# Kernel optimization log

Hardware: AMD Instinct MI355X
Metric: run time of the kernel (lower is better)

## Reference

```python
import jax, jax.numpy as jnp
import numpy as np
import math

N_HEAD = 4
NORM_GROUPS = 32
EPS = 1e-5


def setup_inputs() -> dict:
    key = jax.random.key(0)
    ks = jax.random.split(key, 6)
    C = 256
    x = jax.random.normal(ks[0], (2, C, 64, 64), dtype=jnp.float32)
    gn_w = jnp.ones((C,), dtype=jnp.float32)
    gn_b = jnp.zeros((C,), dtype=jnp.float32)
    s = 1.0 / math.sqrt(C)
    wq = jax.random.normal(ks[1], (C, C), dtype=jnp.float32) * s
    wk = jax.random.normal(ks[2], (C, C), dtype=jnp.float32) * s
    wv = jax.random.normal(ks[3], (C, C), dtype=jnp.float32) * s
    wo = jax.random.normal(ks[4], (C, C), dtype=jnp.float32) * s
    bo = jnp.zeros((C,), dtype=jnp.float32)
    return {"x": x, "gn_w": gn_w, "gn_b": gn_b, "wq": wq, "wk": wk,
            "wv": wv, "wo": wo, "bo": bo}


def group_norm(x, w, b):
    bsz, c, h, wd = x.shape
    xg = x.reshape(bsz, NORM_GROUPS, c // NORM_GROUPS, h, wd)
    mu = jnp.mean(xg, axis=(2, 3, 4), keepdims=True)
    var = jnp.mean(jnp.square(xg - mu), axis=(2, 3, 4), keepdims=True)
    xn = ((xg - mu) * jax.lax.rsqrt(var + EPS)).reshape(bsz, c, h, wd)
    return xn * w[None, :, None, None] + b[None, :, None, None]


def conv1x1(x, w):
    # w: (out_ch, in_ch) applied pointwise
    return jnp.einsum('bchw,oc->bohw', x, w)


def reference(x, gn_w, gn_b, wq, wk, wv, wo, bo):
    bsz, c, h, w = x.shape
    hd = c // N_HEAD
    norm = group_norm(x, gn_w, gn_b)
    q = conv1x1(norm, wq).reshape(bsz, N_HEAD, hd, h, w)
    k = conv1x1(norm, wk).reshape(bsz, N_HEAD, hd, h, w)
    v = conv1x1(norm, wv).reshape(bsz, N_HEAD, hd, h, w)
    # scores over full spatial positions; NOTE: scaled by sqrt(channel), as in source
    scores = jnp.einsum('bnchw,bncxy->bnhwxy', q, k) / jnp.sqrt(jnp.float32(c))
    probs = jax.nn.softmax(scores.reshape(bsz, N_HEAD, h, w, h * w), axis=-1)
    probs = probs.reshape(bsz, N_HEAD, h, w, h, w)
    out = jnp.einsum('bnhwxy,bncxy->bnchw', probs, v).reshape(bsz, c, h, w)
    out = conv1x1(out, wo) + bo[None, :, None, None]
    return out + x
```

## Files before the change

### kernel.cpp

```cpp
#include <hip/hip_runtime.h>

typedef float f32x4 __attribute__((ext_vector_type(4)));
typedef float f32x16 __attribute__((ext_vector_type(16)));
typedef short bf16x8 __attribute__((ext_vector_type(8)));
typedef unsigned short u16;
typedef unsigned int u32;

#define MFMA(a, b, c) __builtin_amdgcn_mfma_f32_16x16x32_bf16((a), (b), (c), 0, 0, 0)
#define MFMA32(a, b, c) __builtin_amdgcn_mfma_f32_32x32x16_bf16((a), (b), (c), 0, 0, 0)

static __device__ __forceinline__ u16 f2bf(float f) {
    union { float f; u32 u; } v; v.f = f;
    u32 r = v.u + 0x7FFFu + ((v.u >> 16) & 1u);
    return (u16)(r >> 16);
}

static __device__ __forceinline__ u32 pkbf(float a, float b) {
    u32 ua = __float_as_uint(a) + 0x8000u;
    u32 ub = __float_as_uint(b) + 0x8000u;
    return __builtin_amdgcn_perm(ub, ua, 0x07060302);
}

__global__ __launch_bounds__(256) void wcvt_kernel(
    const float* __restrict__ wq, const float* __restrict__ wk,
    const float* __restrict__ wv, const float* __restrict__ wo,
    u16* __restrict__ Wbf) {
    int base = (blockIdx.x * 256 + threadIdx.x) * 4;
    int p = base >> 16;
    int off = base & 65535;
    const float* W = (p == 0) ? wq : ((p == 1) ? wk : ((p == 2) ? wv : wo));
    float sc = (p == 0) ? 0.0625f : 1.0f;
    float4 v = *(const float4*)(W + off);
    uint2 pk;
    pk.x = pkbf(v.x * sc, v.y * sc);
    pk.y = pkbf(v.z * sc, v.w * sc);
    *(uint2*)(Wbf + base) = pk;
}

__global__ __launch_bounds__(256) void gn_stats(
    const float* __restrict__ x, float2* __restrict__ part) {
    int blk = blockIdx.x;
    int bg = blk >> 2, quarter = blk & 3;
    const float* xp = x + (size_t)bg * 32768 + quarter * 8192;
    int t = threadIdx.x;

    float s = 0.f, ss = 0.f;
#pragma unroll
    for (int rep = 0; rep < 8; ++rep) {
        float4 v = *(const float4*)(xp + t * 4 + rep * 1024);
        s += v.x + v.y + v.z + v.w;
        ss += v.x * v.x + v.y * v.y + v.z * v.z + v.w * v.w;
    }
    for (int off = 1; off < 64; off <<= 1) {
        s += __shfl_xor(s, off);
        ss += __shfl_xor(ss, off);
    }
    __shared__ float red[8];
    int lane = t & 63, w = t >> 6;
    if (lane == 0) { red[w] = s; red[4 + w] = ss; }
    __syncthreads();
    if (t == 0) {
        part[blk] = make_float2(red[0] + red[1] + red[2] + red[3],
                                red[4] + red[5] + red[6] + red[7]);
    }
}

__global__ __launch_bounds__(256) void gn_apply(
    const float* __restrict__ x, const float* __restrict__ gw,
    const float* __restrict__ gb, const float2* __restrict__ part,
    u16* __restrict__ normT) {
    int s0 = blockIdx.x * 32;
    int b = blockIdx.y;
    int t = threadIdx.x;
    __shared__ u16 tile[32 * 264];
    __shared__ float2 gstat[32];

    if (t < 32) {
        float s = 0.f, ss = 0.f;
#pragma unroll
        for (int q = 0; q < 4; ++q) {
            float2 p = part[(b * 32 + t) * 4 + q];
            s += p.x; ss += p.y;
        }
        float mu = s * (1.f / 32768.f);
        float var = ss * (1.f / 32768.f) - mu * mu;
        gstat[t] = make_float2(mu, rsqrtf(var + 1e-5f));
    }
    __syncthreads();

    int sj = (t & 7) * 4;
#pragma unroll
    for (int i = 0; i < 8; ++i) {
        int c = (t >> 3) + 32 * i;
        float2 st = gstat[c >> 3];
        float wgt = gw[c] * st.y;
        float bia = gb[c] - st.x * wgt;
        float4 v = *(const float4*)(x + (size_t)(b * 256 + c) * 4096 + s0 + sj);
        tile[(sj + 0) * 264 + c] = f2bf(v.x * wgt + bia);
        tile[(sj + 1) * 264 + c] = f2bf(v.y * wgt + bia);
        tile[(sj + 2) * 264 + c] = f2bf(v.z * wgt + bia);
        tile[(sj + 3) * 264 + c] = f2bf(v.w * wgt + bia);
    }
    __syncthreads();
#pragma unroll
    for (int k = 0; k < 4; ++k) {
        int idx = t + 256 * k;
        int row = idx >> 5, ch = idx & 31;
        *(uint4*)(normT + ((size_t)(b * 4096 + s0 + row)) * 256 + ch * 8) =
            *(const uint4*)(tile + row * 264 + ch * 8);
    }
}

__global__ __launch_bounds__(256) void qkv_gemm(
    const u16* __restrict__ normT, const u16* __restrict__ Wbf,
    u16* __restrict__ Q, u16* __restrict__ K, u16* __restrict__ V) {
    int b = blockIdx.y & 1;
    int p = blockIdx.y >> 1;
    const u16* W = Wbf + p * 65536;
    int m0 = (blockIdx.x & 1) * 128;
    int n0 = (blockIdx.x >> 1) * 64;

    __shared__ u16 a_s[128 * 40];
    __shared__ u16 b_s[64 * 40];

    int t = threadIdx.x;
    int lane = t & 63, wave = t >> 6;
    int wm = wave & 1, wn = wave >> 1;
    int r = lane & 15, qd = lane >> 4;

    const u16* Bsrc = normT + (size_t)b * 4096 * 256;

    f32x4 acc[4][2];
#pragma unroll
    for (int i = 0; i < 4; ++i)
#pragma unroll
        for (int j = 0; j < 2; ++j) acc[i][j] = (f32x4){0.f, 0.f, 0.f, 0.f};

    int srow = t >> 1;
    int scp = (t & 1) * 16;

    for (int kk = 0; kk < 256; kk += 32) {
        __syncthreads();
        {
            const u16* src = W + (m0 + srow) * 256 + kk + scp;
            *(uint4*)(a_s + srow * 40 + scp) = *(const uint4*)(src);
            *(uint4*)(a_s + srow * 40 + scp + 8) = *(const uint4*)(src + 8);
        }
        if (t < 128) {
            const u16* src = Bsrc + (size_t)(n0 + srow) * 256 + kk + scp;
            *(uint4*)(b_s + srow * 40 + scp) = *(const uint4*)(src);
            *(uint4*)(b_s + srow * 40 + scp + 8) = *(const uint4*)(src + 8);
        }
        __syncthreads();

        bf16x8 af[4], bf[2];
#pragma unroll
        for (int mt = 0; mt < 4; ++mt)
            af[mt] = *(const bf16x8*)(a_s + (wm * 64 + mt * 16 + r) * 40 + qd * 8);
#pragma unroll
        for (int nt = 0; nt < 2; ++nt)
            bf[nt] = *(const bf16x8*)(b_s + (wn * 32 + nt * 16 + r) * 40 + qd * 8);
        if (p == 2) {
#pragma unroll
            for (int mt = 0; mt < 4; ++mt)
#pragma unroll
                for (int nt = 0; nt < 2; ++nt)
                    acc[mt][nt] = MFMA(bf[nt], af[mt], acc[mt][nt]);
        } else {
#pragma unroll
            for (int mt = 0; mt < 4; ++mt)
#pragma unroll
                for (int nt = 0; nt < 2; ++nt)
                    acc[mt][nt] = MFMA(af[mt], bf[nt], acc[mt][nt]);
        }
    }

    if (p < 2) {
        u16* dst = (p == 0) ? Q : K;
#pragma unroll
        for (int mt = 0; mt < 4; ++mt) {
#pragma unroll
            for (int nt = 0; nt < 2; ++nt) {
                int o0 = m0 + wm * 64 + mt * 16 + qd * 4;
                int s = n0 + wn * 32 + nt * 16 + r;
                int h = o0 >> 6, d0 = o0 & 63;
                uint2 pk;
                pk.x = pkbf(acc[mt][nt][0], acc[mt][nt][1]);
                pk.y = pkbf(acc[mt][nt][2], acc[mt][nt][3]);
                *(uint2*)(dst + ((size_t)((b * 4 + h) * 4096 + s)) * 64 + d0) = pk;
            }
        }
    } else {
#pragma unroll
        for (int mt = 0; mt < 4; ++mt) {
#pragma unroll
            for (int nt = 0; nt < 2; ++nt) {
                int o = m0 + wm * 64 + mt * 16 + r;
                int h = o >> 6, d = o & 63;
                int sb = n0 + wn * 32 + nt * 16 + qd * 4;
                uint2 pk;
                pk.x = pkbf(acc[mt][nt][0], acc[mt][nt][1]);
                pk.y = pkbf(acc[mt][nt][2], acc[mt][nt][3]);
                *(uint2*)(V + ((size_t)((b * 4 + h) * 64 + d)) * 4096 + sb) = pk;
            }
        }
    }
}

template <int QT>
__global__ __launch_bounds__(256, 2) void attn_kernel(
    const u16* __restrict__ Q, const u16* __restrict__ K,
    const u16* __restrict__ V, u16* __restrict__ Opart,
    float* __restrict__ Lpart, int nk32) {
    int bh = blockIdx.x & 7, sp = blockIdx.x >> 3;
    int qb = blockIdx.y;
    int t = threadIdx.x, lane = t & 63, w = t >> 6;
    int qn = lane & 31, h = lane >> 5;

    const size_t bhoff = (size_t)bh * 4096 * 64;
    int q0 = (qb * 4 + w) * (32 * QT);
    int kbase = sp * nk32 * 32;

    bf16x8 qf[QT][4];
#pragma unroll
    for (int qt = 0; qt < QT; ++qt)
#pragma unroll
        for (int c = 0; c < 4; ++c)
            qf[qt][c] = *(const bf16x8*)(Q + bhoff +
                (size_t)(q0 + qt * 32 + qn) * 64 + c * 16 + h * 8);

    f32x16 oacc[2][QT];
#pragma unroll
    for (int dt = 0; dt < 2; ++dt)
#pragma unroll
        for (int qt = 0; qt < QT; ++qt)
#pragma unroll
            for (int i = 0; i < 16; ++i) oacc[dt][qt][i] = 0.f;
    float lacc[QT];
#pragma unroll
    for (int qt = 0; qt < QT; ++qt) lacc[qt] = 0.f;

    const u16* Kp = K + bhoff;
    const u16* Vp = V + bhoff;

    for (int kt = 0; kt < nk32; ++kt) {
        int k0 = kbase + kt * 32;
        bf16x8 kf[4];
#pragma unroll
        for (int c = 0; c < 4; ++c)
            kf[c] = *(const bf16x8*)(Kp + (size_t)(k0 + qn) * 64 + c * 16 + h * 8);
        bf16x8 vf[2][2];
#pragma unroll
        for (int dt = 0; dt < 2; ++dt)
#pragma unroll
            for (int kc = 0; kc < 2; ++kc)
                vf[dt][kc] = *(const bf16x8*)(Vp +
                    (size_t)(dt * 32 + qn) * 4096 + k0 + kc * 16 + h * 8);

#pragma unroll
        for (int qt = 0; qt < QT; ++qt) {
            f32x16 s;
#pragma unroll
            for (int i = 0; i < 16; ++i) s[i] = 0.f;
#pragma unroll
            for (int c = 0; c < 4; ++c) s = MFMA32(kf[c], qf[qt][c], s);

            float e[16];
            float ls = 0.f;
#pragma unroll
            for (int i = 0; i < 16; ++i) { e[i] = __expf(s[i]); ls += e[i]; }
            lacc[qt] += ls;

            u32 p[8], rm[8];
#pragma unroll
            for (int i = 0; i < 8; ++i) p[i] = pkbf(e[2 * i], e[2 * i + 1]);
#pragma unroll
            for (int i = 0; i < 8; ++i)
                rm[i] = (u32)__shfl_xor((int)p[i], 32);

            u32 a0 = h ? rm[2] : p[0], a1 = h ? rm[3] : p[1];
            u32 a2 = h ? p[2] : rm[0], a3 = h ? p[3] : rm[1];
            u32 b0 = h ? rm[6] : p[4], b1 = h ? rm[7] : p[5];
            u32 b2 = h ? p[6] : rm[4], b3 = h ? p[7] : rm[5];
            uint4 pau = {a0, a1, a2, a3};
            uint4 pbu = {b0, b1, b2, b3};
            bf16x8 pA = *(const bf16x8*)&pau;
            bf16x8 pB = *(const bf16x8*)&pbu;

#pragma unroll
            for (int dt = 0; dt < 2; ++dt) {
                oacc[dt][qt] = MFMA32(vf[dt][0], pA, oacc[dt][qt]);
                oacc[dt][qt] = MFMA32(vf[dt][1], pB, oacc[dt][qt]);
            }
        }
    }

    float lfull[QT];
#pragma unroll
    for (int qt = 0; qt < QT; ++qt)
        lfull[qt] = lacc[qt] + __shfl_xor(lacc[qt], 32);

    __shared__ u16 osw[4][64 * 72];
    u16* my = osw[w];
#pragma unroll
    for (int qt = 0; qt < QT; ++qt) {
        int row = qt * 32 + qn;
#pragma unroll
        for (int dt = 0; dt < 2; ++dt) {
#pragma unroll
            for (int g = 0; g < 4; ++g) {
                int d0 = g * 8 + h * 4 + dt * 32;
                uint2 pk;
                pk.x = pkbf(oacc[dt][qt][4 * g], oacc[dt][qt][4 * g + 1]);
                pk.y = pkbf(oacc[dt][qt][4 * g + 2], oacc[dt][qt][4 * g + 3]);
                *(uint2*)(my + row * 72 + d0) = pk;
            }
        }
    }
    __syncthreads();

    size_t obase = ((size_t)sp * 8 + bh) * 4096 + q0;
#pragma unroll
    for (int rr = 0; rr < 4 * QT; ++rr) {
        int row = rr * 8 + (lane >> 3), ch = lane & 7;
        uint4 v = *(const uint4*)(my + row * 72 + ch * 8);
        *(uint4*)(Opart + (obase + row) * 64 + ch * 8) = v;
    }
    if (h == 0) {
#pragma unroll
        for (int qt = 0; qt < QT; ++qt)
            Lpart[obase + qt * 32 + qn] = lfull[qt];
    }
}

__global__ __launch_bounds__(256) void attn_combine(
    const u16* __restrict__ Opart, const float* __restrict__ Lpart,
    u16* __restrict__ attnT, int nsplit) {
    int t = threadIdx.x;
    int gr = blockIdx.x * 64 + (t >> 2);
    int d0 = (t & 3) * 16;

    float l = 0.f;
    for (int s = 0; s < nsplit; ++s) l += Lpart[(size_t)s * 32768 + gr];
    float inv = 1.f / l;

    float acc[16];
#pragma unroll
    for (int i = 0; i < 16; ++i) acc[i] = 0.f;
    for (int s = 0; s < nsplit; ++s) {
        const u16* p = Opart + ((size_t)s * 32768 + gr) * 64 + d0;
        uint4 a = *(const uint4*)(p);
        uint4 bq = *(const uint4*)(p + 8);
        const u32* ap = (const u32*)&a;
        const u32* bp = (const u32*)&bq;
#pragma unroll
        for (int j = 0; j < 4; ++j) {
            acc[2 * j]     += __uint_as_float(ap[j] << 16);
            acc[2 * j + 1] += __uint_as_float(ap[j] & 0xFFFF0000u);
            acc[8 + 2 * j]     += __uint_as_float(bp[j] << 16);
            acc[8 + 2 * j + 1] += __uint_as_float(bp[j] & 0xFFFF0000u);
        }
    }
    u32 pk[8];
#pragma unroll
    for (int j = 0; j < 8; ++j)
        pk[j] = pkbf(acc[2 * j] * inv, acc[2 * j + 1] * inv);

    int bh = gr >> 12, q = gr & 4095;
    int b = bh >> 2, hh = bh & 3;
    u16* dst = attnT + ((size_t)(b * 4096 + q)) * 256 + hh * 64 + d0;
    *(uint4*)(dst) = make_uint4(pk[0], pk[1], pk[2], pk[3]);
    *(uint4*)(dst + 8) = make_uint4(pk[4], pk[5], pk[6], pk[7]);
}

__global__ __launch_bounds__(256) void out_gemm(
    const u16* __restrict__ attnT, const u16* __restrict__ W3,
    const float* __restrict__ bo, const float* __restrict__ x,
    float* __restrict__ out) {
    int b = blockIdx.y;
    int m0 = (blockIdx.x & 3) * 64;
    int n0 = (blockIdx.x >> 2) * 64;

    __shared__ u16 a_s[64 * 40];
    __shared__ u16 b_s[64 * 40];

    int t = threadIdx.x;
    int lane = t & 63, wave = t >> 6;
    int wm = wave & 1, wn = wave >> 1;
    int r = lane & 15, qd = lane >> 4;

    const u16* Bsrc = attnT + (size_t)b * 4096 * 256;

    f32x4 acc[2][2];
#pragma unroll
    for (int i = 0; i < 2; ++i)
#pragma unroll
        for (int j = 0; j < 2; ++j) acc[i][j] = (f32x4){0.f, 0.f, 0.f, 0.f};

    int u = t & 127;
    int srow = u >> 1;
    int scp = (u & 1) * 16;

    for (int kk = 0; kk < 256; kk += 32) {
        __syncthreads();
        if (t < 128) {
            const u16* src = W3 + (m0 + srow) * 256 + kk + scp;
            *(uint4*)(a_s + srow * 40 + scp) = *(const uint4*)(src);
            *(uint4*)(a_s + srow * 40 + scp + 8) = *(const uint4*)(src + 8);
        } else {
            const u16* src = Bsrc + (size_t)(n0 + srow) * 256 + kk + scp;
            *(uint4*)(b_s + srow * 40 + scp) = *(const uint4*)(src);
            *(uint4*)(b_s + srow * 40 + scp + 8) = *(const uint4*)(src + 8);
        }
        __syncthreads();

        bf16x8 af[2], bf[2];
#pragma unroll
        for (int mt = 0; mt < 2; ++mt)
            af[mt] = *(const bf16x8*)(a_s + (wm * 32 + mt * 16 + r) * 40 + qd * 8);
#pragma unroll
        for (int nt = 0; nt < 2; ++nt)
            bf[nt] = *(const bf16x8*)(b_s + (wn * 32 + nt * 16 + r) * 40 + qd * 8);
#pragma unroll
        for (int mt = 0; mt < 2; ++mt)
#pragma unroll
            for (int nt = 0; nt < 2; ++nt)
                acc[mt][nt] = MFMA(af[mt], bf[nt], acc[mt][nt]);
    }

#pragma unroll
    for (int mt = 0; mt < 2; ++mt) {
#pragma unroll
        for (int nt = 0; nt < 2; ++nt) {
#pragma unroll
            for (int j = 0; j < 4; ++j) {
                int o = m0 + wm * 32 + mt * 16 + qd * 4 + j;
                int s = n0 + wn * 32 + nt * 16 + r;
                size_t idx = (size_t)(b * 256 + o) * 4096 + s;
                out[idx] = acc[mt][nt][j] + bo[o] + x[idx];
            }
        }
    }
}

extern "C" void kernel_launch(void* const* d_in, const int* in_sizes, int n_in,
                              void* d_out, int out_size, void* d_ws, size_t ws_size,
                              hipStream_t stream) {
    const float* x = (const float*)d_in[0];
    const float* gn_w = (const float*)d_in[1];
    const float* gn_b = (const float*)d_in[2];
    const float* wq = (const float*)d_in[3];
    const float* wk = (const float*)d_in[4];
    const float* wv = (const float*)d_in[5];
    const float* wo = (const float*)d_in[6];
    const float* bo = (const float*)d_in[7];
    float* out = (float*)d_out;

    char* ws = (char*)d_ws;
    u16* normT = (u16*)(ws);
    u16* attnT = (u16*)(ws);
    u16* Q     = (u16*)(ws + (4u << 20));
    u16* Kp    = (u16*)(ws + (8u << 20));
    u16* Vp    = (u16*)(ws + (12u << 20));
    u16* Wbf   = (u16*)(ws + (16u << 20));
    float2* part = (float2*)(ws + (16u << 20) + 524288);

    size_t opart_off = (size_t)17 << 20;
    size_t opart_bytes4 = 4ull * 8 * 4096 * 64 * 2;
    int nsplit = (ws_size >= opart_off + opart_bytes4 + 4ull * 32768 * 4 + 4096)
                     ? 4 : 2;
    u16* Opart = (u16*)(ws + opart_off);
    float* Lpart = (float*)(ws + opart_off + (size_t)nsplit * 8 * 4096 * 64 * 2);

    wcvt_kernel<<<256, 256, 0, stream>>>(wq, wk, wv, wo, Wbf);
    gn_stats<<<256, 256, 0, stream>>>(x, part);
    gn_apply<<<dim3(128, 2), 256, 0, stream>>>(x, gn_w, gn_b, part, normT);
    qkv_gemm<<<dim3(128, 6), 256, 0, stream>>>(normT, Wbf, Q, Kp, Vp);
    if (nsplit == 4) {
        attn_kernel<2><<<dim3(32, 16), 256, 0, stream>>>(Q, Kp, Vp, Opart, Lpart, 32);
    } else {
        attn_kernel<1><<<dim3(16, 32), 256, 0, stream>>>(Q, Kp, Vp, Opart, Lpart, 64);
    }
    attn_combine<<<512, 256, 0, stream>>>(Opart, Lpart, attnT, nsplit);
    out_gemm<<<dim3(256, 2), 256, 0, stream>>>(attnT, Wbf + 3 * 65536, bo, x, out);
}
```

Measured before the change: 172.7 us.

## Fuse weight conversion and split-combine into GEMMs, double-buffer KV loads in attention

Removes the separate weight-conversion kernel by converting fp32 weights to bf16 inside the QKV and output GEMM tile loads. Removes the attn_combine kernel by summing split partial outputs and normalizing inside the output GEMM's B-tile load. In attention, K/V fragments are loaded one step ahead into ping-pong register buffers, and the V load is changed to strided uint2 loads, which removes the cross-lane shuffle that rearranged P. Fewer launches and intermediate buffers are traded for redundant weight conversion per block and extra register pressure.

```diff
diff --git a/kernel.cpp b/kernel.cpp
--- a/kernel.cpp
+++ b/kernel.cpp
@@ -21,20 +21,9 @@
     return __builtin_amdgcn_perm(ub, ua, 0x07060302);
 }
 
-__global__ __launch_bounds__(256) void wcvt_kernel(
-    const float* __restrict__ wq, const float* __restrict__ wk,
-    const float* __restrict__ wv, const float* __restrict__ wo,
-    u16* __restrict__ Wbf) {
-    int base = (blockIdx.x * 256 + threadIdx.x) * 4;
-    int p = base >> 16;
-    int off = base & 65535;
-    const float* W = (p == 0) ? wq : ((p == 1) ? wk : ((p == 2) ? wv : wo));
-    float sc = (p == 0) ? 0.0625f : 1.0f;
-    float4 v = *(const float4*)(W + off);
-    uint2 pk;
-    pk.x = pkbf(v.x * sc, v.y * sc);
-    pk.y = pkbf(v.z * sc, v.w * sc);
-    *(uint2*)(Wbf + base) = pk;
+static __device__ __forceinline__ bf16x8 mk8(uint2 a, uint2 b) {
+    uint4 t = {a.x, a.y, b.x, b.y};
+    return *(const bf16x8*)&t;
 }
 
 __global__ __launch_bounds__(256) void gn_stats(
@@ -112,11 +101,13 @@
 }
 
 __global__ __launch_bounds__(256) void qkv_gemm(
-    const u16* __restrict__ normT, const u16* __restrict__ Wbf,
+    const u16* __restrict__ normT, const float* __restrict__ wq,
+    const float* __restrict__ wk, const float* __restrict__ wv,
     u16* __restrict__ Q, u16* __restrict__ K, u16* __restrict__ V) {
     int b = blockIdx.y & 1;
     int p = blockIdx.y >> 1;
-    const u16* W = Wbf + p * 65536;
+    const float* W = (p == 0) ? wq : ((p == 1) ? wk : wv);
+    float sc = (p == 0) ? 0.0625f : 1.0f;
     int m0 = (blockIdx.x & 1) * 128;
     int n0 = (blockIdx.x >> 1) * 64;
 
@@ -142,9 +133,22 @@
     for (int kk = 0; kk < 256; kk += 32) {
         __syncthreads();
         {
-            const u16* src = W + (m0 + srow) * 256 + kk + scp;
-            *(uint4*)(a_s + srow * 40 + scp) = *(const uint4*)(src);
-            *(uint4*)(a_s + srow * 40 + scp + 8) = *(const uint4*)(src + 8);
+            const float* src = W + (m0 + srow) * 256 + kk + scp;
+            float4 f0 = *(const float4*)(src + 0);
+            float4 f1 = *(const float4*)(src + 4);
+            float4 f2 = *(const float4*)(src + 8);
+            float4 f3 = *(const float4*)(src + 12);
+            uint4 o0, o1;
+            o0.x = pkbf(f0.x * sc, f0.y * sc);
+            o0.y = pkbf(f0.z * sc, f0.w * sc);
+            o0.z = pkbf(f1.x * sc, f1.y * sc);
+            o0.w = pkbf(f1.z * sc, f1.w * sc);
+            o1.x = pkbf(f2.x * sc, f2.y * sc);
+            o1.y = pkbf(f2.z * sc, f2.w * sc);
+            o1.z = pkbf(f3.x * sc, f3.y * sc);
+            o1.w = pkbf(f3.z * sc, f3.w * sc);
+            *(uint4*)(a_s + srow * 40 + scp) = o0;
+            *(uint4*)(a_s + srow * 40 + scp + 8) = o1;
         }
         if (t < 128) {
             const u16* src = Bsrc + (size_t)(n0 + srow) * 256 + kk + scp;
@@ -207,6 +211,25 @@
     }
 }
 
+struct KVfrag {
+    bf16x8 kf[4];
+    bf16x8 vf[2][2];
+};
+
+static __device__ __forceinline__ void load_kv(
+    KVfrag& o, const u16* __restrict__ Kp, const u16* __restrict__ Vp,
+    int k0, int qn, int h) {
+#pragma unroll
+    for (int c = 0; c < 4; ++c)
+        o.kf[c] = *(const bf16x8*)(Kp + (size_t)(k0 + qn) * 64 + c * 16 + h * 8);
+#pragma unroll
+    for (int dt = 0; dt < 2; ++dt) {
+        const u16* vr = Vp + (size_t)(dt * 32 + qn) * 4096 + k0 + 4 * h;
+        o.vf[dt][0] = mk8(*(const uint2*)(vr), *(const uint2*)(vr + 8));
+        o.vf[dt][1] = mk8(*(const uint2*)(vr + 16), *(const uint2*)(vr + 24));
+    }
+}
+
 template <int QT>
 __global__ __launch_bounds__(256, 2) void attn_kernel(
     const u16* __restrict__ Q, const u16* __restrict__ K,
@@ -243,27 +266,17 @@
     const u16* Kp = K + bhoff;
     const u16* Vp = V + bhoff;
 
-    for (int kt = 0; kt < nk32; ++kt) {
-        int k0 = kbase + kt * 32;
-        bf16x8 kf[4];
-#pragma unroll
-        for (int c = 0; c < 4; ++c)
-            kf[c] = *(const bf16x8*)(Kp + (size_t)(k0 + qn) * 64 + c * 16 + h * 8);
-        bf16x8 vf[2][2];
-#pragma unroll
-        for (int dt = 0; dt < 2; ++dt)
-#pragma unroll
-            for (int kc = 0; kc < 2; ++kc)
-                vf[dt][kc] = *(const bf16x8*)(Vp +
-                    (size_t)(dt * 32 + qn) * 4096 + k0 + kc * 16 + h * 8);
-
+    KVfrag buf0, buf1;
+    load_kv(buf0, Kp, Vp, kbase, qn, h);
+
+    auto step = [&](const KVfrag& kv) {
 #pragma unroll
         for (int qt = 0; qt < QT; ++qt) {
             f32x16 s;
 #pragma unroll
             for (int i = 0; i < 16; ++i) s[i] = 0.f;
 #pragma unroll
-            for (int c = 0; c < 4; ++c) s = MFMA32(kf[c], qf[qt][c], s);
+            for (int c = 0; c < 4; ++c) s = MFMA32(kv.kf[c], qf[qt][c], s);
 
             float e[16];
             float ls = 0.f;
@@ -271,28 +284,28 @@
             for (int i = 0; i < 16; ++i) { e[i] = __expf(s[i]); ls += e[i]; }
             lacc[qt] += ls;
 
-            u32 p[8], rm[8];
+            u32 p[8];
 #pragma unroll
             for (int i = 0; i < 8; ++i) p[i] = pkbf(e[2 * i], e[2 * i + 1]);
-#pragma unroll
-            for (int i = 0; i < 8; ++i)
-                rm[i] = (u32)__shfl_xor((int)p[i], 32);
-
-            u32 a0 = h ? rm[2] : p[0], a1 = h ? rm[3] : p[1];
-            u32 a2 = h ? p[2] : rm[0], a3 = h ? p[3] : rm[1];
-            u32 b0 = h ? rm[6] : p[4], b1 = h ? rm[7] : p[5];
-            u32 b2 = h ? p[6] : rm[4], b3 = h ? p[7] : rm[5];
-            uint4 pau = {a0, a1, a2, a3};
-            uint4 pbu = {b0, b1, b2, b3};
-            bf16x8 pA = *(const bf16x8*)&pau;
-            bf16x8 pB = *(const bf16x8*)&pbu;
+            uint4 pa = {p[0], p[1], p[2], p[3]};
+            uint4 pb = {p[4], p[5], p[6], p[7]};
+            bf16x8 pA = *(const bf16x8*)&pa;
+            bf16x8 pB = *(const bf16x8*)&pb;
 
 #pragma unroll
             for (int dt = 0; dt < 2; ++dt) {
-                oacc[dt][qt] = MFMA32(vf[dt][0], pA, oacc[dt][qt]);
-                oacc[dt][qt] = MFMA32(vf[dt][1], pB, oacc[dt][qt]);
+                oacc[dt][qt] = MFMA32(kv.vf[dt][0], pA, oacc[dt][qt]);
+                oacc[dt][qt] = MFMA32(kv.vf[dt][1], pB, oacc[dt][qt]);
             }
         }
+    };
+
+    for (int kt = 0; kt < nk32; kt += 2) {
+        load_kv(buf1, Kp, Vp, kbase + (kt + 1) * 32, qn, h);
+        step(buf0);
+        int k2 = (kt + 2 < nk32) ? kbase + (kt + 2) * 32 : kbase;
+        load_kv(buf0, Kp, Vp, k2, qn, h);
+        step(buf1);
     }
 
     float lfull[QT];
@@ -333,63 +346,30 @@
     }
 }
 
-__global__ __launch_bounds__(256) void attn_combine(
+__global__ __launch_bounds__(256) void out_gemm(
     const u16* __restrict__ Opart, const float* __restrict__ Lpart,
-    u16* __restrict__ attnT, int nsplit) {
-    int t = threadIdx.x;
-    int gr = blockIdx.x * 64 + (t >> 2);
-    int d0 = (t & 3) * 16;
-
-    float l = 0.f;
-    for (int s = 0; s < nsplit; ++s) l += Lpart[(size_t)s * 32768 + gr];
-    float inv = 1.f / l;
-
-    float acc[16];
-#pragma unroll
-    for (int i = 0; i < 16; ++i) acc[i] = 0.f;
-    for (int s = 0; s < nsplit; ++s) {
-        const u16* p = Opart + ((size_t)s * 32768 + gr) * 64 + d0;
-        uint4 a = *(const uint4*)(p);
-        uint4 bq = *(const uint4*)(p + 8);
-        const u32* ap = (const u32*)&a;
-        const u32* bp = (const u32*)&bq;
-#pragma unroll
-        for (int j = 0; j < 4; ++j) {
-            acc[2 * j]     += __uint_as_float(ap[j] << 16);
-            acc[2 * j + 1] += __uint_as_float(ap[j] & 0xFFFF0000u);
-            acc[8 + 2 * j]     += __uint_as_float(bp[j] << 16);
-            acc[8 + 2 * j + 1] += __uint_as_float(bp[j] & 0xFFFF0000u);
-        }
-    }
-    u32 pk[8];
-#pragma unroll
-    for (int j = 0; j < 8; ++j)
-        pk[j] = pkbf(acc[2 * j] * inv, acc[2 * j + 1] * inv);
-
-    int bh = gr >> 12, q = gr & 4095;
-    int b = bh >> 2, hh = bh & 3;
-    u16* dst = attnT + ((size_t)(b * 4096 + q)) * 256 + hh * 64 + d0;
-    *(uint4*)(dst) = make_uint4(pk[0], pk[1], pk[2], pk[3]);
-    *(uint4*)(dst + 8) = make_uint4(pk[4], pk[5], pk[6], pk[7]);
-}
-
-__global__ __launch_bounds__(256) void out_gemm(
-    const u16* __restrict__ attnT, const u16* __restrict__ W3,
-    const float* __restrict__ bo, const float* __restrict__ x,
-    float* __restrict__ out) {
+    const float* __restrict__ wo, const float* __restrict__ bo,
+    const float* __restrict__ x, float* __restrict__ out, int nsplit) {
     int b = blockIdx.y;
     int m0 = (blockIdx.x & 3) * 64;
     int n0 = (blockIdx.x >> 2) * 64;
 
     __shared__ u16 a_s[64 * 40];
     __shared__ u16 b_s[64 * 40];
+    __shared__ float il[4][64];
 
     int t = threadIdx.x;
     int lane = t & 63, wave = t >> 6;
     int wm = wave & 1, wn = wave >> 1;
     int r = lane & 15, qd = lane >> 4;
 
-    const u16* Bsrc = attnT + (size_t)b * 4096 * 256;
+    {
+        int hh = t >> 6, j = t & 63;
+        float l = 0.f;
+        for (int s = 0; s < nsplit; ++s)
+            l += Lpart[((size_t)s * 8 + b * 4 + hh) * 4096 + n0 + j];
+        il[hh][j] = 1.f / l;
+    }
 
     f32x4 acc[2][2];
 #pragma unroll
@@ -404,13 +384,51 @@
     for (int kk = 0; kk < 256; kk += 32) {
         __syncthreads();
         if (t < 128) {
-            const u16* src = W3 + (m0 + srow) * 256 + kk + scp;
-            *(uint4*)(a_s + srow * 40 + scp) = *(const uint4*)(src);
-            *(uint4*)(a_s + srow * 40 + scp + 8) = *(const uint4*)(src + 8);
+            const float* src = wo + (m0 + srow) * 256 + kk + scp;
+            float4 f0 = *(const float4*)(src + 0);
+            float4 f1 = *(const float4*)(src + 4);
+            float4 f2 = *(const float4*)(src + 8);
+            float4 f3 = *(const float4*)(src + 12);
+            uint4 o0, o1;
+            o0.x = pkbf(f0.x, f0.y); o0.y = pkbf(f0.z, f0.w);
+            o0.z = pkbf(f1.x, f1.y); o0.w = pkbf(f1.z, f1.w);
+            o1.x = pkbf(f2.x, f2.y); o1.y = pkbf(f2.z, f2.w);
+            o1.z = pkbf(f3.x, f3.y); o1.w = pkbf(f3.z, f3.w);
+            *(uint4*)(a_s + srow * 40 + scp) = o0;
+            *(uint4*)(a_s + srow * 40 + scp + 8) = o1;
         } else {
-            const u16* src = Bsrc + (size_t)(n0 + srow) * 256 + kk + scp;
-            *(uint4*)(b_s + srow * 40 + scp) = *(const uint4*)(src);
-            *(uint4*)(b_s + srow * 40 + scp + 8) = *(const uint4*)(src + 8);
+            int hc = kk >> 6;
+            int dbase = (kk & 63) + scp;
+            float av[16];
+#pragma unroll
+            for (int i = 0; i < 16; ++i) av[i] = 0.f;
+            for (int s = 0; s < nsplit; ++s) {
+                const u16* p = Opart +
+                    (((size_t)s * 8 + b * 4 + hc) * 4096 + n0 + srow) * 64 + dbase;
+                uint4 A = *(const uint4*)(p);
+                uint4 B = *(const uint4*)(p + 8);
+                const u32* ap = (const u32*)&A;
+                const u32* bp = (const u32*)&B;
+#pragma unroll
+                for (int j = 0; j < 4; ++j) {
+                    av[2 * j]     += __uint_as_float(ap[j] << 16);
+                    av[2 * j + 1] += __uint_as_float(ap[j] & 0xFFFF0000u);
+                    av[8 + 2 * j]     += __uint_as_float(bp[j] << 16);
+                    av[8 + 2 * j + 1] += __uint_as_float(bp[j] & 0xFFFF0000u);
+                }
+            }
+            float sc = il[hc][srow];
+            uint4 o0, o1;
+            o0.x = pkbf(av[0] * sc, av[1] * sc);
+            o0.y = pkbf(av[2] * sc, av[3] * sc);
+            o0.z = pkbf(av[4] * sc, av[5] * sc);
+            o0.w = pkbf(av[6] * sc, av[7] * sc);
+            o1.x = pkbf(av[8] * sc, av[9] * sc);
+            o1.y = pkbf(av[10] * sc, av[11] * sc);
+            o1.z = pkbf(av[12] * sc, av[13] * sc);
+            o1.w = pkbf(av[14] * sc, av[15] * sc);
+            *(uint4*)(b_s + srow * 40 + scp) = o0;
+            *(uint4*)(b_s + srow * 40 + scp + 8) = o1;
         }
         __syncthreads();
 
@@ -458,12 +476,10 @@
 
     char* ws = (char*)d_ws;
     u16* normT = (u16*)(ws);
-    u16* attnT = (u16*)(ws);
     u16* Q     = (u16*)(ws + (4u << 20));
     u16* Kp    = (u16*)(ws + (8u << 20));
     u16* Vp    = (u16*)(ws + (12u << 20));
-    u16* Wbf   = (u16*)(ws + (16u << 20));
-    float2* part = (float2*)(ws + (16u << 20) + 524288);
+    float2* part = (float2*)(ws + (16u << 20));
 
     size_t opart_off = (size_t)17 << 20;
     size_t opart_bytes4 = 4ull * 8 * 4096 * 64 * 2;
@@ -472,15 +488,13 @@
     u16* Opart = (u16*)(ws + opart_off);
     float* Lpart = (float*)(ws + opart_off + (size_t)nsplit * 8 * 4096 * 64 * 2);
 
-    wcvt_kernel<<<256, 256, 0, stream>>>(wq, wk, wv, wo, Wbf);
     gn_stats<<<256, 256, 0, stream>>>(x, part);
     gn_apply<<<dim3(128, 2), 256, 0, stream>>>(x, gn_w, gn_b, part, normT);
-    qkv_gemm<<<dim3(128, 6), 256, 0, stream>>>(normT, Wbf, Q, Kp, Vp);
+    qkv_gemm<<<dim3(128, 6), 256, 0, stream>>>(normT, wq, wk, wv, Q, Kp, Vp);
     if (nsplit == 4) {
         attn_kernel<2><<<dim3(32, 16), 256, 0, stream>>>(Q, Kp, Vp, Opart, Lpart, 32);
     } else {
         attn_kernel<1><<<dim3(16, 32), 256, 0, stream>>>(Q, Kp, Vp, Opart, Lpart, 64);
     }
-    attn_combine<<<512, 256, 0, stream>>>(Opart, Lpart, attnT, nsplit);
-    out_gemm<<<dim3(256, 2), 256, 0, stream>>>(attnT, Wbf + 3 * 65536, bo, x, out);
-}
+    out_gemm<<<dim3(256, 2), 256, 0, stream>>>(Opart, Lpart, wo, bo, x, out, nsplit);
+}
```

Result: slower. 208.8 us (+20.9%).
